# Optimization experiments

Hardware: AMD Instinct MI355X
Metric: run time of the kernel (lower is better)

Reference implementation:

```python
import jax, jax.numpy as jnp
import numpy as np

KK = 9  # 3x3 kernel taps
BN_EPS = 1e-5


def setup_inputs() -> dict:
    key = jax.random.key(0)
    ks = jax.random.split(key, 8)
    B, C, H, W = 2, 64, 256, 256
    O = 64
    x = jax.random.normal(ks[0], (B, C, H, W), dtype=jnp.float32)
    # offset/mask conv: 3*KK output channels (dy[9], dx[9], mask[9])
    w_off = jax.random.normal(ks[1], (3 * KK, C, 3, 3), dtype=jnp.float32) * 0.05
    b_off = jnp.zeros((3 * KK,), dtype=jnp.float32)
    # deformable conv weight
    w = jax.random.normal(ks[2], (O, C, 3, 3), dtype=jnp.float32) * (1.0 / np.sqrt(C * KK))
    b = jnp.zeros((O,), dtype=jnp.float32)
    gamma = jnp.ones((O,), dtype=jnp.float32)
    beta = jnp.zeros((O,), dtype=jnp.float32)
    return {"x": x, "w_off": w_off, "b_off": b_off, "w": w, "b": b,
            "gamma": gamma, "beta": beta}


def _dcn_bn_act_res(x, w_off, b_off, w, b, gamma, beta):
    B, C, H, W = x.shape
    O = w.shape[0]
    # offset/mask prediction via plain 3x3 conv
    om = jax.lax.conv_general_dilated(
        x, w_off, window_strides=(1, 1), padding=[(1, 1), (1, 1)],
        dimension_numbers=("NCHW", "OIHW", "NCHW")) + b_off[None, :, None, None]
    off_y = om[:, :KK]            # [B,9,H,W]
    off_x = om[:, KK:2 * KK]      # [B,9,H,W]
    mask = jax.nn.sigmoid(om[:, 2 * KK:])  # [B,9,H,W] modulation

    # absolute sampling coordinates: base grid + kernel tap offset (-1..1) + learned offset
    ky, kx = jnp.meshgrid(jnp.arange(3), jnp.arange(3), indexing="ij")
    ky = ky.reshape(KK).astype(jnp.float32) - 1.0
    kx = kx.reshape(KK).astype(jnp.float32) - 1.0
    hs = jnp.arange(H, dtype=jnp.float32)
    ws = jnp.arange(W, dtype=jnp.float32)
    py = off_y + hs[None, None, :, None] + ky[None, :, None, None]  # [B,9,H,W]
    px = off_x + ws[None, None, None, :] + kx[None, :, None, None]

    y0 = jnp.floor(py)
    x0 = jnp.floor(px)
    wy = py - y0
    wx = px - x0
    y0i = y0.astype(jnp.int32)
    x0i = x0.astype(jnp.int32)

    def gather(img, yi, xi):
        # img [C,H,W], yi/xi [9,H,W]; zero outside (implicit zero padding)
        valid = (yi >= 0) & (yi < H) & (xi >= 0) & (xi < W)
        yc = jnp.clip(yi, 0, H - 1)
        xc = jnp.clip(xi, 0, W - 1)
        return img[:, yc, xc] * valid[None].astype(img.dtype)  # [C,9,H,W]

    def sample_one(img, yi, xi, wy_, wx_):
        v00 = gather(img, yi, xi)
        v01 = gather(img, yi, xi + 1)
        v10 = gather(img, yi + 1, xi)
        v11 = gather(img, yi + 1, xi + 1)
        w00 = ((1 - wy_) * (1 - wx_))[None]
        w01 = ((1 - wy_) * wx_)[None]
        w10 = (wy_ * (1 - wx_))[None]
        w11 = (wy_ * wx_)[None]
        return v00 * w00 + v01 * w01 + v10 * w10 + v11 * w11  # [C,9,H,W]

    sampled = jax.vmap(sample_one)(x, y0i, x0i, wy, wx)  # [B,C,9,H,W]
    sampled = sampled * mask[:, None]

    out = jnp.einsum("bckhw,ock->bohw", sampled, w.reshape(O, C, KK))
    out = out + b[None, :, None, None]

    # BatchNorm (training-mode batch statistics)
    mu = out.mean(axis=(0, 2, 3), keepdims=True)
    var = out.var(axis=(0, 2, 3), keepdims=True)
    out = (out - mu) * jax.lax.rsqrt(var + BN_EPS)
    out = out * gamma[None, :, None, None] + beta[None, :, None, None]

    return jax.nn.relu(out) + x  # residual


def reference(x, w_off, b_off, w, b, gamma, beta):
    return _dcn_bn_act_res(x, w_off, b_off, w, b, gamma, beta)
```

## Files before the change

kernel.cpp:

```cpp
#include <hip/hip_runtime.h>
#include <hip/hip_fp16.h>
#include <math.h>

#define HWSZ 65536
#define IMGH 256
#define IMGW 256

typedef _Float16 half8 __attribute__((ext_vector_type(8)));
typedef float f32x4 __attribute__((ext_vector_type(4)));

__device__ inline unsigned short f2bf(float f) {
    unsigned u = __float_as_uint(f);
    return (unsigned short)((u + 0x7fffu + ((u >> 16) & 1u)) >> 16);
}
__device__ inline unsigned short f2h(float f) {
    __half h = __float2half(f);
    return __half_as_ushort(h);
}
__device__ inline __half2 duph2(unsigned s) {
    union { unsigned u; __half2 h; } c;
    c.u = (s & 0xffffu) * 0x10001u;
    return c.h;
}
__device__ inline void hacc(const uint4& q, __half2 w, __half2* v) {
    const __half2* h = (const __half2*)&q;
    v[0] = __hfma2(h[0], w, v[0]);
    v[1] = __hfma2(h[1], w, v[1]);
    v[2] = __hfma2(h[2], w, v[2]);
    v[3] = __hfma2(h[3], w, v[3]);
}

__global__ void prep_weights(const float* __restrict__ w_off,
                             const float* __restrict__ w,
                             unsigned short* __restrict__ wApack,
                             unsigned short* __restrict__ wOffPack) {
    int i = blockIdx.x * 256 + threadIdx.x;
    if (i < 36864) {
        int e = i;
        int j = e & 7, lane = (e >> 3) & 63, kk = (e >> 9) & 1;
        int t2 = e >> 10;
        int tap = t2 % 9, g = t2 / 9;
        int o = g * 16 + (lane & 15);
        int c = kk * 32 + ((lane >> 4) & 3) * 8 + j;
        wApack[e] = f2h(w[(o * 64 + c) * 9 + tap]);
    } else if (i < 36864 + 18432) {
        int e = i - 36864;
        int j = e & 7, lane = (e >> 3) & 63, kk = (e >> 9) & 1;
        int t2 = e >> 10;
        int tap = t2 % 9, mt = t2 / 9;
        int d = mt * 16 + (lane & 15);
        int c = kk * 32 + ((lane >> 4) & 3) * 8 + j;
        float v = (d < 27) ? w_off[(d * 64 + c) * 9 + tap] : 0.f;
        wOffPack[e] = f2h(v);
    }
}

__global__ __launch_bounds__(256) void transpose_x(const float* __restrict__ x,
                                                   unsigned short* __restrict__ xT) {
    __shared__ float tile[64 * 65];
    int blk = blockIdx.x;
    int b = blk >> 10;
    int p0 = (blk & 1023) * 64;
    int t = threadIdx.x;
    const float* xb = x + (size_t)b * 64 * HWSZ;
    unsigned short* xTb = xT + (size_t)b * HWSZ * 64;
    int pp = t & 63;
    int c0r = t >> 6;
#pragma unroll
    for (int i = 0; i < 16; ++i) {
        int c = c0r + 4 * i;
        tile[c * 65 + pp] = xb[(size_t)c * HWSZ + p0 + pp];
    }
    __syncthreads();
#pragma unroll
    for (int it = 0; it < 2; ++it) {
        int item = t + it * 256;
        int p = item >> 3;
        int c0 = (item & 7) * 8;
        uint4 ow;
        ow.x = f2h(tile[(c0 + 0) * 65 + p]) | ((unsigned)f2h(tile[(c0 + 1) * 65 + p]) << 16);
        ow.y = f2h(tile[(c0 + 2) * 65 + p]) | ((unsigned)f2h(tile[(c0 + 3) * 65 + p]) << 16);
        ow.z = f2h(tile[(c0 + 4) * 65 + p]) | ((unsigned)f2h(tile[(c0 + 5) * 65 + p]) << 16);
        ow.w = f2h(tile[(c0 + 6) * 65 + p]) | ((unsigned)f2h(tile[(c0 + 7) * 65 + p]) << 16);
        *(uint4*)&xTb[(size_t)(p0 + p) * 64 + c0] = ow;
    }
}

__global__ __launch_bounds__(256) void offset_conv(const unsigned short* __restrict__ xT,
                                                   const unsigned short* __restrict__ wOffPack,
                                                   const float* __restrict__ b_off,
                                                   float* __restrict__ om) {
    __shared__ uint4 haloBuf[800];
    char* halo = (char*)haloBuf;
    int bid = blockIdx.x;
    int blk = ((bid & 7) << 8) | (bid >> 3);
    int b = blk >> 10;
    int tb = blk & 1023;
    int ty = tb >> 5, tx = tb & 31;
    int h0 = ty * 8, w0 = tx * 8;
    int t = threadIdx.x;
    const char* xbb = (const char*)(xT + (size_t)b * HWSZ * 64);

    for (int i = t; i < 800; i += 256) {
        int cell = i >> 3;
        int c0 = (i & 7) * 8;
        int r = cell / 10, s = cell - r * 10;
        int y = h0 - 1 + r, xx = w0 - 1 + s;
        uint4 v = {0u, 0u, 0u, 0u};
        if (y >= 0 && y < IMGH && xx >= 0 && xx < IMGW)
            v = *(const uint4*)(xbb + ((size_t)(y * IMGW + xx) << 7) + (c0 << 1));
        *(uint4*)(halo + (cell << 7) + (((c0 << 1)) ^ ((cell & 7) << 4))) = v;
    }
    __syncthreads();

    int lane = t & 63;
    int wid = __builtin_amdgcn_readfirstlane(t >> 6);
    int mt = wid & 1;
    int np = wid >> 1;
    f32x4 z = {0.f, 0.f, 0.f, 0.f};
    f32x4 acc[2] = {z, z};
    int lhi = lane >> 4;

    for (int tap = 0; tap < 9; ++tap) {
        const half8* ap = (const half8*)wOffPack;
        half8 a0 = ap[((mt * 9 + tap) * 2 + 0) * 64 + lane];
        half8 a1 = ap[((mt * 9 + tap) * 2 + 1) * 64 + lane];
        int dy = tap / 3, dx = tap - dy * 3;
#pragma unroll
        for (int nn = 0; nn < 2; ++nn) {
            int p = (np * 2 + nn) * 16 + (lane & 15);
            int cell = ((p >> 3) + dy) * 10 + (p & 7) + dx;
            int base = (cell << 7);
            int swz = (cell & 7) << 4;
            half8 b0 = *(const half8*)(halo + base + ((lhi << 4) ^ swz));
            acc[nn] = __builtin_amdgcn_mfma_f32_16x16x32_f16(a0, b0, acc[nn], 0, 0, 0);
            half8 b1 = *(const half8*)(halo + base + (((4 + lhi) << 4) ^ swz));
            acc[nn] = __builtin_amdgcn_mfma_f32_16x16x32_f16(a1, b1, acc[nn], 0, 0, 0);
        }
    }
    float* omb = om + (size_t)b * 27 * HWSZ;
#pragma unroll
    for (int nn = 0; nn < 2; ++nn) {
#pragma unroll
        for (int jj = 0; jj < 4; ++jj) {
            int d = mt * 16 + lhi * 4 + jj;
            if (d < 27) {
                int p = (np * 2 + nn) * 16 + (lane & 15);
                int gp = (h0 + (p >> 3)) * IMGW + w0 + (p & 7);
                omb[(size_t)d * HWSZ + gp] = acc[nn][jj] + b_off[d];
            }
        }
    }
}

__global__ __launch_bounds__(512, 4) void dcn_main(const unsigned short* __restrict__ xT,
                                                   const float* __restrict__ om,
                                                   const unsigned short* __restrict__ wApack,
                                                   unsigned short* __restrict__ preout,
                                                   float* __restrict__ stats) {
    __shared__ uint4 haloBuf[3744];
    __shared__ unsigned prmi[9][128];
    __shared__ uint2 prmw[9][128];
    __shared__ float bstats[128];
    char* halo = (char*)haloBuf;
    int bid = blockIdx.x;
    int blk = ((bid & 7) << 7) | (bid >> 3);
    int b = blk >> 9;
    int tb = blk & 511;
    int ty = tb >> 5, tx = tb & 31;
    int h0 = ty * 16, w0 = tx * 8;
    int t = threadIdx.x;
    const char* xbb = (const char*)(xT + (size_t)b * HWSZ * 64);
    const float* omb = om + (size_t)b * 27 * HWSZ;
    int lane = t & 63;
    int wid = t >> 6;
    int lp = lane & 15;
    int lhi = lane >> 4;
    int p = wid * 16 + lp;
    int hb = h0 - 5, wb = w0 - 5;

    if (t < 128) bstats[t] = 0.f;

    for (int i = t; i < 3744; i += 512) {
        int cell = i >> 3;
        int ch = i & 7;
        int r = cell / 18, c = cell - r * 18;
        int y = hb + r, xx = wb + c;
        uint4 v = {0u, 0u, 0u, 0u};
        if ((unsigned)y < 256u && (unsigned)xx < 256u)
            v = *(const uint4*)(xbb + ((size_t)((y << 8) + xx) << 7) + (ch << 4));
        *(uint4*)(halo + (cell << 7) + ((ch ^ (cell & 7)) << 4)) = v;
    }

    for (int i = t; i < 1152; i += 512) {
        int tap = i >> 7, pp = i & 127;
        int h = h0 + (pp >> 3), wc = w0 + (pp & 7);
        int gp = h * IMGW + wc;
        float offy = omb[(size_t)tap * HWSZ + gp];
        float offx = omb[(size_t)(tap + 9) * HWSZ + gp];
        float mraw = omb[(size_t)(tap + 18) * HWSZ + gp];
        float m = 1.f / (1.f + __expf(-mraw));
        float pyf = (float)(h + tap / 3 - 1) + offy;
        float pxf = (float)(wc + tap % 3 - 1) + offx;
        float y0f = floorf(pyf), x0f = floorf(pxf);
        float wy = pyf - y0f, wx = pxf - x0f;
        int y0 = (int)y0f, x0 = (int)x0f;
        int y1 = y0 + 1, x1 = x0 + 1;
        float vy0 = (y0 >= 0 && y0 < IMGH) ? 1.f : 0.f;
        float vy1 = (y1 >= 0 && y1 < IMGH) ? 1.f : 0.f;
        float vx0 = (x0 >= 0 && x0 < IMGW) ? 1.f : 0.f;
        float vx1 = (x1 >= 0 && x1 < IMGW) ? 1.f : 0.f;
        float w00 = (1.f - wy) * (1.f - wx) * m * vy0 * vx0;
        float w01 = (1.f - wy) * wx * m * vy0 * vx1;
        float w10 = wy * (1.f - wx) * m * vy1 * vx0;
        float w11 = wy * wx * m * vy1 * vx1;
        prmw[tap][pp] = make_uint2((unsigned)f2h(w00) | ((unsigned)f2h(w01) << 16),
                                   (unsigned)f2h(w10) | ((unsigned)f2h(w11) << 16));
        int ry0 = y0 - hb, rx0 = x0 - wb;
        unsigned enc;
        if ((unsigned)ry0 <= 24u && (unsigned)rx0 <= 16u) {
            enc = (unsigned)((ry0 * 18 + rx0) << 7);
        } else {
            int y0s = min(max(y0, -8), 383) + 8;
            int x0s = min(max(x0, -8), 383) + 8;
            enc = 1u | ((unsigned)y0s << 1) | ((unsigned)x0s << 10);
        }
        prmi[tap][pp] = enc;
    }
    __syncthreads();

    f32x4 z = {0.f, 0.f, 0.f, 0.f};
    f32x4 acc[4] = {z, z, z, z};
    const half8* ap = (const half8*)wApack;
    uint4 q[4][2];

#define LOADC(PI)                                                             \
    {                                                                         \
        unsigned pi_ = (PI);                                                  \
        bool fb_ = (pi_ & 1u);                                                \
        unsigned base_ = fb_ ? 0u : pi_;                                      \
        unsigned o00 = base_, o01 = base_ + 128u,                             \
                 o10 = base_ + 2304u, o11 = base_ + 2432u;                    \
        q[0][0] = *(const uint4*)(halo + o00 + ((lhi ^ ((o00 >> 7) & 7)) << 4));       \
        q[0][1] = *(const uint4*)(halo + o00 + (((4 + lhi) ^ ((o00 >> 7) & 7)) << 4)); \
        q[1][0] = *(const uint4*)(halo + o01 + ((lhi ^ ((o01 >> 7) & 7)) << 4));       \
        q[1][1] = *(const uint4*)(halo + o01 + (((4 + lhi) ^ ((o01 >> 7) & 7)) << 4)); \
        q[2][0] = *(const uint4*)(halo + o10 + ((lhi ^ ((o10 >> 7) & 7)) << 4));       \
        q[2][1] = *(const uint4*)(halo + o10 + (((4 + lhi) ^ ((o10 >> 7) & 7)) << 4)); \
        q[3][0] = *(const uint4*)(halo + o11 + ((lhi ^ ((o11 >> 7) & 7)) << 4));       \
        q[3][1] = *(const uint4*)(halo + o11 + (((4 + lhi) ^ ((o11 >> 7) & 7)) << 4)); \
        if (__ballot(fb_)) {                                                  \
            if (fb_) {                                                        \
                int y0r = (int)((pi_ >> 1) & 511) - 8;                        \
                int x0r = (int)((pi_ >> 10) & 511) - 8;                       \
                int y0c = min(max(y0r, 0), 255), y1c = min(max(y0r + 1, 0), 255); \
                int x0c = min(max(x0r, 0), 255), x1c = min(max(x0r + 1, 0), 255); \
                const char* g00 = xbb + (((y0c << 8) + x0c) << 7) + (lhi << 4); \
                const char* g01 = xbb + (((y0c << 8) + x1c) << 7) + (lhi << 4); \
                const char* g10 = xbb + (((y1c << 8) + x0c) << 7) + (lhi << 4); \
                const char* g11 = xbb + (((y1c << 8) + x1c) << 7) + (lhi << 4); \
                q[0][0] = *(const uint4*)g00; q[0][1] = *(const uint4*)(g00 + 64); \
                q[1][0] = *(const uint4*)g01; q[1][1] = *(const uint4*)(g01 + 64); \
                q[2][0] = *(const uint4*)g10; q[2][1] = *(const uint4*)(g10 + 64); \
                q[3][0] = *(const uint4*)g11; q[3][1] = *(const uint4*)(g11 + 64); \
            }                                                                 \
        }                                                                     \
    }

    unsigned pi = prmi[0][p];
    uint2 ww = prmw[0][p];
    LOADC(pi);

#pragma unroll
    for (int tap = 0; tap < 9; ++tap) {
        __half2 W00 = duph2(ww.x), W01 = duph2(ww.x >> 16);
        __half2 W10 = duph2(ww.y), W11 = duph2(ww.y >> 16);
        union HV { __half2 h2[4]; half8 h8; } V0, V1;
        __half2 z2 = __float2half2_rn(0.f);
#pragma unroll
        for (int j = 0; j < 4; ++j) { V0.h2[j] = z2; V1.h2[j] = z2; }
        hacc(q[0][0], W00, V0.h2); hacc(q[0][1], W00, V1.h2);
        hacc(q[1][0], W01, V0.h2); hacc(q[1][1], W01, V1.h2);
        hacc(q[2][0], W10, V0.h2); hacc(q[2][1], W10, V1.h2);
        hacc(q[3][0], W11, V0.h2); hacc(q[3][1], W11, V1.h2);
        half8 b0 = V0.h8, b1 = V1.h8;
        if (tap < 8) {
            pi = prmi[tap + 1][p];
            ww = prmw[tap + 1][p];
            LOADC(pi);
        }
        __builtin_amdgcn_s_setprio(1);
#pragma unroll
        for (int g2 = 0; g2 < 4; ++g2) {
            half8 a0 = ap[((g2 * 9 + tap) * 2 + 0) * 64 + lane];
            half8 a1 = ap[((g2 * 9 + tap) * 2 + 1) * 64 + lane];
            acc[g2] = __builtin_amdgcn_mfma_f32_16x16x32_f16(a0, b0, acc[g2], 0, 0, 0);
            acc[g2] = __builtin_amdgcn_mfma_f32_16x16x32_f16(a1, b1, acc[g2], 0, 0, 0);
        }
        __builtin_amdgcn_s_setprio(0);
    }
#undef LOADC

    unsigned short* pob = preout + (size_t)b * 64 * HWSZ;
    int gp = (h0 + (p >> 3)) * IMGW + w0 + (p & 7);
#pragma unroll
    for (int g2 = 0; g2 < 4; ++g2) {
#pragma unroll
        for (int jj = 0; jj < 4; ++jj) {
            int o = g2 * 16 + lhi * 4 + jj;
            pob[(size_t)o * HWSZ + gp] = f2bf(acc[g2][jj]);
        }
    }
#pragma unroll
    for (int g2 = 0; g2 < 4; ++g2) {
#pragma unroll
        for (int jj = 0; jj < 4; ++jj) {
            float s1 = acc[g2][jj];
            float s2 = s1 * s1;
#pragma unroll
            for (int mask = 1; mask < 16; mask <<= 1) {
                s1 += __shfl_xor(s1, mask);
                s2 += __shfl_xor(s2, mask);
            }
            if (lp == 0) {
                int o = g2 * 16 + lhi * 4 + jj;
                atomicAdd(&bstats[o], s1);
                atomicAdd(&bstats[64 + o], s2);
            }
        }
    }
    __syncthreads();
    if (t < 128) atomicAdd(&stats[t], bstats[t]);
}

__global__ __launch_bounds__(256) void bn_finalize(const float* __restrict__ stats,
                                                   const float* __restrict__ gamma,
                                                   const float* __restrict__ beta,
                                                   const float* __restrict__ x,
                                                   const unsigned short* __restrict__ preout,
                                                   float* __restrict__ out) {
    int i = blockIdx.x * 256 + threadIdx.x;
    int e0 = i * 8;
    int o = (e0 >> 16) & 63;
    const float inv_n = 1.f / 131072.f;
    float mean = stats[o] * inv_n;
    float var = stats[64 + o] * inv_n - mean * mean;
    float rstd = rsqrtf(var + 1e-5f);
    float g = gamma[o] * rstd;
    float bb = beta[o] - mean * g;
    uint4 q = ((const uint4*)preout)[i];
    float4 x0 = ((const float4*)x)[i * 2];
    float4 x1 = ((const float4*)x)[i * 2 + 1];
    float4 r0, r1;
    r0.x = fmaxf(__uint_as_float(q.x << 16) * g + bb, 0.f) + x0.x;
    r0.y = fmaxf(__uint_as_float(q.x & 0xffff0000u) * g + bb, 0.f) + x0.y;
    r0.z = fmaxf(__uint_as_float(q.y << 16) * g + bb, 0.f) + x0.z;
    r0.w = fmaxf(__uint_as_float(q.y & 0xffff0000u) * g + bb, 0.f) + x0.w;
    r1.x = fmaxf(__uint_as_float(q.z << 16) * g + bb, 0.f) + x1.x;
    r1.y = fmaxf(__uint_as_float(q.z & 0xffff0000u) * g + bb, 0.f) + x1.y;
    r1.z = fmaxf(__uint_as_float(q.w << 16) * g + bb, 0.f) + x1.z;
    r1.w = fmaxf(__uint_as_float(q.w & 0xffff0000u) * g + bb, 0.f) + x1.w;
    ((float4*)out)[i * 2] = r0;
    ((float4*)out)[i * 2 + 1] = r1;
}

extern "C" void kernel_launch(void* const* d_in, const int* in_sizes, int n_in,
                              void* d_out, int out_size, void* d_ws, size_t ws_size,
                              hipStream_t stream) {
    const float* x     = (const float*)d_in[0];
    const float* w_off = (const float*)d_in[1];
    const float* b_off = (const float*)d_in[2];
    const float* w     = (const float*)d_in[3];
    const float* gamma = (const float*)d_in[5];
    const float* beta  = (const float*)d_in[6];
    float* out = (float*)d_out;
    char* wsb = (char*)d_ws;

    unsigned short* xT       = (unsigned short*)wsb;
    float*          om       = (float*)(wsb + 16777216);
    unsigned short* preout   = (unsigned short*)(wsb + 30932992);
    unsigned short* wApack   = (unsigned short*)(wsb + 47710208);
    unsigned short* wOffPack = (unsigned short*)(wsb + 47783936);
    float*          stats    = (float*)(wsb + 47820800);

    hipMemsetAsync(stats, 0, 512, stream);
    prep_weights<<<216, 256, 0, stream>>>(w_off, w, wApack, wOffPack);
    transpose_x<<<2048, 256, 0, stream>>>(x, xT);
    offset_conv<<<2048, 256, 0, stream>>>(xT, wOffPack, b_off, om);
    dcn_main<<<1024, 512, 0, stream>>>(xT, om, wApack, preout, stats);
    bn_finalize<<<4096, 256, 0, stream>>>(stats, gamma, beta, x, preout, out);
}
```

Baseline: 101.6 us.

## Fuse offset/mask convolution into main DCN kernel using the shared halo tile

Removes the separate offset_conv kernel and computes the 27-channel offset/mask conv inside dcn_main from the already-loaded 5-pixel halo, writing results to shared memory instead of a global om buffer. Per-pixel sampling indices and bilinear weights are now held in registers (9 entries per thread) rather than in shared arrays, and halo addressing is simplified to a cell index with XOR swizzle. This eliminates a kernel launch and a ~14MB global round trip for om, at the cost of extra registers and MFMA work inside the main kernel, which may reduce occupancy.

Result: slower. 104.1 us (+2.4%).

```diff
diff --git a/kernel.cpp b/kernel.cpp
--- a/kernel.cpp
+++ b/kernel.cpp
@@ -86,81 +86,14 @@
     }
 }
 
-__global__ __launch_bounds__(256) void offset_conv(const unsigned short* __restrict__ xT,
+__global__ __launch_bounds__(512, 4) void dcn_main(const unsigned short* __restrict__ xT,
+                                                   const unsigned short* __restrict__ wApack,
                                                    const unsigned short* __restrict__ wOffPack,
                                                    const float* __restrict__ b_off,
-                                                   float* __restrict__ om) {
-    __shared__ uint4 haloBuf[800];
-    char* halo = (char*)haloBuf;
-    int bid = blockIdx.x;
-    int blk = ((bid & 7) << 8) | (bid >> 3);
-    int b = blk >> 10;
-    int tb = blk & 1023;
-    int ty = tb >> 5, tx = tb & 31;
-    int h0 = ty * 8, w0 = tx * 8;
-    int t = threadIdx.x;
-    const char* xbb = (const char*)(xT + (size_t)b * HWSZ * 64);
-
-    for (int i = t; i < 800; i += 256) {
-        int cell = i >> 3;
-        int c0 = (i & 7) * 8;
-        int r = cell / 10, s = cell - r * 10;
-        int y = h0 - 1 + r, xx = w0 - 1 + s;
-        uint4 v = {0u, 0u, 0u, 0u};
-        if (y >= 0 && y < IMGH && xx >= 0 && xx < IMGW)
-            v = *(const uint4*)(xbb + ((size_t)(y * IMGW + xx) << 7) + (c0 << 1));
-        *(uint4*)(halo + (cell << 7) + (((c0 << 1)) ^ ((cell & 7) << 4))) = v;
-    }
-    __syncthreads();
-
-    int lane = t & 63;
-    int wid = __builtin_amdgcn_readfirstlane(t >> 6);
-    int mt = wid & 1;
-    int np = wid >> 1;
-    f32x4 z = {0.f, 0.f, 0.f, 0.f};
-    f32x4 acc[2] = {z, z};
-    int lhi = lane >> 4;
-
-    for (int tap = 0; tap < 9; ++tap) {
-        const half8* ap = (const half8*)wOffPack;
-        half8 a0 = ap[((mt * 9 + tap) * 2 + 0) * 64 + lane];
-        half8 a1 = ap[((mt * 9 + tap) * 2 + 1) * 64 + lane];
-        int dy = tap / 3, dx = tap - dy * 3;
-#pragma unroll
-        for (int nn = 0; nn < 2; ++nn) {
-            int p = (np * 2 + nn) * 16 + (lane & 15);
-            int cell = ((p >> 3) + dy) * 10 + (p & 7) + dx;
-            int base = (cell << 7);
-            int swz = (cell & 7) << 4;
-            half8 b0 = *(const half8*)(halo + base + ((lhi << 4) ^ swz));
-            acc[nn] = __builtin_amdgcn_mfma_f32_16x16x32_f16(a0, b0, acc[nn], 0, 0, 0);
-            half8 b1 = *(const half8*)(halo + base + (((4 + lhi) << 4) ^ swz));
-            acc[nn] = __builtin_amdgcn_mfma_f32_16x16x32_f16(a1, b1, acc[nn], 0, 0, 0);
-        }
-    }
-    float* omb = om + (size_t)b * 27 * HWSZ;
-#pragma unroll
-    for (int nn = 0; nn < 2; ++nn) {
-#pragma unroll
-        for (int jj = 0; jj < 4; ++jj) {
-            int d = mt * 16 + lhi * 4 + jj;
-            if (d < 27) {
-                int p = (np * 2 + nn) * 16 + (lane & 15);
-                int gp = (h0 + (p >> 3)) * IMGW + w0 + (p & 7);
-                omb[(size_t)d * HWSZ + gp] = acc[nn][jj] + b_off[d];
-            }
-        }
-    }
-}
-
-__global__ __launch_bounds__(512, 4) void dcn_main(const unsigned short* __restrict__ xT,
-                                                   const float* __restrict__ om,
-                                                   const unsigned short* __restrict__ wApack,
                                                    unsigned short* __restrict__ preout,
                                                    float* __restrict__ stats) {
     __shared__ uint4 haloBuf[3744];
-    __shared__ unsigned prmi[9][128];
-    __shared__ uint2 prmw[9][128];
+    __shared__ float om_s[27 * 128];
     __shared__ float bstats[128];
     char* halo = (char*)haloBuf;
     int bid = blockIdx.x;
@@ -171,11 +104,11 @@
     int h0 = ty * 16, w0 = tx * 8;
     int t = threadIdx.x;
     const char* xbb = (const char*)(xT + (size_t)b * HWSZ * 64);
-    const float* omb = om + (size_t)b * 27 * HWSZ;
     int lane = t & 63;
     int wid = t >> 6;
     int lp = lane & 15;
     int lhi = lane >> 4;
+    unsigned lhi16 = (unsigned)(lhi << 4);
     int p = wid * 16 + lp;
     int hb = h0 - 5, wb = w0 - 5;
 
@@ -191,68 +124,101 @@
             v = *(const uint4*)(xbb + ((size_t)((y << 8) + xx) << 7) + (ch << 4));
         *(uint4*)(halo + (cell << 7) + ((ch ^ (cell & 7)) << 4)) = v;
     }
-
-    for (int i = t; i < 1152; i += 512) {
-        int tap = i >> 7, pp = i & 127;
-        int h = h0 + (pp >> 3), wc = w0 + (pp & 7);
-        int gp = h * IMGW + wc;
-        float offy = omb[(size_t)tap * HWSZ + gp];
-        float offx = omb[(size_t)(tap + 9) * HWSZ + gp];
-        float mraw = omb[(size_t)(tap + 18) * HWSZ + gp];
-        float m = 1.f / (1.f + __expf(-mraw));
-        float pyf = (float)(h + tap / 3 - 1) + offy;
-        float pxf = (float)(wc + tap % 3 - 1) + offx;
-        float y0f = floorf(pyf), x0f = floorf(pxf);
-        float wy = pyf - y0f, wx = pxf - x0f;
-        int y0 = (int)y0f, x0 = (int)x0f;
-        int y1 = y0 + 1, x1 = x0 + 1;
-        float vy0 = (y0 >= 0 && y0 < IMGH) ? 1.f : 0.f;
-        float vy1 = (y1 >= 0 && y1 < IMGH) ? 1.f : 0.f;
-        float vx0 = (x0 >= 0 && x0 < IMGW) ? 1.f : 0.f;
-        float vx1 = (x1 >= 0 && x1 < IMGW) ? 1.f : 0.f;
-        float w00 = (1.f - wy) * (1.f - wx) * m * vy0 * vx0;
-        float w01 = (1.f - wy) * wx * m * vy0 * vx1;
-        float w10 = wy * (1.f - wx) * m * vy1 * vx0;
-        float w11 = wy * wx * m * vy1 * vx1;
-        prmw[tap][pp] = make_uint2((unsigned)f2h(w00) | ((unsigned)f2h(w01) << 16),
-                                   (unsigned)f2h(w10) | ((unsigned)f2h(w11) << 16));
-        int ry0 = y0 - hb, rx0 = x0 - wb;
-        unsigned enc;
-        if ((unsigned)ry0 <= 24u && (unsigned)rx0 <= 16u) {
-            enc = (unsigned)((ry0 * 18 + rx0) << 7);
-        } else {
-            int y0s = min(max(y0, -8), 383) + 8;
-            int x0s = min(max(x0, -8), 383) + 8;
-            enc = 1u | ((unsigned)y0s << 1) | ((unsigned)x0s << 10);
-        }
-        prmi[tap][pp] = enc;
-    }
     __syncthreads();
+
+    {
+        int mt = wid & 1;
+        const half8* wp = (const half8*)wOffPack;
+        f32x4 z0 = {0.f, 0.f, 0.f, 0.f};
+#pragma unroll
+        for (int hf = 0; hf < 2; ++hf) {
+            int nt = (wid >> 1) + hf * 4;
+            int pp = nt * 16 + lp;
+            int pr = pp >> 3, pc = pp & 7;
+            f32x4 oa = z0;
+#pragma unroll
+            for (int tap = 0; tap < 9; ++tap) {
+                int dy = tap / 3, dx = tap - dy * 3;
+                int cell = (pr + dy + 4) * 18 + (pc + dx + 4);
+                unsigned ad = (((unsigned)cell << 7) | (((unsigned)cell & 7) << 4)) ^ lhi16;
+                half8 b0 = *(const half8*)(halo + ad);
+                half8 b1 = *(const half8*)(halo + (ad ^ 64u));
+                half8 wa0 = wp[((mt * 9 + tap) * 2 + 0) * 64 + lane];
+                half8 wa1 = wp[((mt * 9 + tap) * 2 + 1) * 64 + lane];
+                oa = __builtin_amdgcn_mfma_f32_16x16x32_f16(wa0, b0, oa, 0, 0, 0);
+                oa = __builtin_amdgcn_mfma_f32_16x16x32_f16(wa1, b1, oa, 0, 0, 0);
+            }
+#pragma unroll
+            for (int jj = 0; jj < 4; ++jj) {
+                int d = mt * 16 + lhi * 4 + jj;
+                if (d < 27) om_s[d * 128 + pp] = oa[jj] + b_off[d];
+            }
+        }
+    }
+    __syncthreads();
+
+    unsigned enc[9];
+    uint2 wwr[9];
+    {
+        int h = h0 + (p >> 3), wc = w0 + (p & 7);
+#pragma unroll
+        for (int tap = 0; tap < 9; ++tap) {
+            float offy = om_s[tap * 128 + p];
+            float offx = om_s[(tap + 9) * 128 + p];
+            float mraw = om_s[(tap + 18) * 128 + p];
+            float m = 1.f / (1.f + __expf(-mraw));
+            float pyf = (float)(h + tap / 3 - 1) + offy;
+            float pxf = (float)(wc + tap % 3 - 1) + offx;
+            float y0f = floorf(pyf), x0f = floorf(pxf);
+            float wy = pyf - y0f, wx = pxf - x0f;
+            int y0 = (int)y0f, x0 = (int)x0f;
+            int y1 = y0 + 1, x1 = x0 + 1;
+            float vy0 = (y0 >= 0 && y0 < IMGH) ? 1.f : 0.f;
+            float vy1 = (y1 >= 0 && y1 < IMGH) ? 1.f : 0.f;
+            float vx0 = (x0 >= 0 && x0 < IMGW) ? 1.f : 0.f;
+            float vx1 = (x1 >= 0 && x1 < IMGW) ? 1.f : 0.f;
+            float w00 = (1.f - wy) * (1.f - wx) * m * vy0 * vx0;
+            float w01 = (1.f - wy) * wx * m * vy0 * vx1;
+            float w10 = wy * (1.f - wx) * m * vy1 * vx0;
+            float w11 = wy * wx * m * vy1 * vx1;
+            wwr[tap] = make_uint2((unsigned)f2h(w00) | ((unsigned)f2h(w01) << 16),
+                                  (unsigned)f2h(w10) | ((unsigned)f2h(w11) << 16));
+            int ry0 = y0 - hb, rx0 = x0 - wb;
+            if ((unsigned)ry0 <= 24u && (unsigned)rx0 <= 16u) {
+                enc[tap] = (unsigned)(ry0 * 18 + rx0) << 1;
+            } else {
+                int y0s = min(max(y0, -8), 383) + 8;
+                int x0s = min(max(x0, -8), 383) + 8;
+                enc[tap] = 1u | ((unsigned)y0s << 1) | ((unsigned)x0s << 10);
+            }
+        }
+    }
 
     f32x4 z = {0.f, 0.f, 0.f, 0.f};
     f32x4 acc[4] = {z, z, z, z};
     const half8* ap = (const half8*)wApack;
     uint4 q[4][2];
 
-#define LOADC(PI)                                                             \
+#define SBASE(CC) ((((CC) << 7) | (((CC) & 7u) << 4)) ^ lhi16)
+#define LOADC(E)                                                              \
     {                                                                         \
-        unsigned pi_ = (PI);                                                  \
-        bool fb_ = (pi_ & 1u);                                                \
-        unsigned base_ = fb_ ? 0u : pi_;                                      \
-        unsigned o00 = base_, o01 = base_ + 128u,                             \
-                 o10 = base_ + 2304u, o11 = base_ + 2432u;                    \
-        q[0][0] = *(const uint4*)(halo + o00 + ((lhi ^ ((o00 >> 7) & 7)) << 4));       \
-        q[0][1] = *(const uint4*)(halo + o00 + (((4 + lhi) ^ ((o00 >> 7) & 7)) << 4)); \
-        q[1][0] = *(const uint4*)(halo + o01 + ((lhi ^ ((o01 >> 7) & 7)) << 4));       \
-        q[1][1] = *(const uint4*)(halo + o01 + (((4 + lhi) ^ ((o01 >> 7) & 7)) << 4)); \
-        q[2][0] = *(const uint4*)(halo + o10 + ((lhi ^ ((o10 >> 7) & 7)) << 4));       \
-        q[2][1] = *(const uint4*)(halo + o10 + (((4 + lhi) ^ ((o10 >> 7) & 7)) << 4)); \
-        q[3][0] = *(const uint4*)(halo + o11 + ((lhi ^ ((o11 >> 7) & 7)) << 4));       \
-        q[3][1] = *(const uint4*)(halo + o11 + (((4 + lhi) ^ ((o11 >> 7) & 7)) << 4)); \
+        unsigned e_ = (E);                                                    \
+        bool fb_ = (e_ & 1u);                                                 \
+        unsigned cl_ = fb_ ? 0u : (e_ >> 1);                                  \
+        unsigned a00 = SBASE(cl_), a01 = SBASE(cl_ + 1u);                     \
+        unsigned a10 = SBASE(cl_ + 18u), a11 = SBASE(cl_ + 19u);              \
+        q[0][0] = *(const uint4*)(halo + a00);                                \
+        q[0][1] = *(const uint4*)(halo + (a00 ^ 64u));                        \
+        q[1][0] = *(const uint4*)(halo + a01);                                \
+        q[1][1] = *(const uint4*)(halo + (a01 ^ 64u));                        \
+        q[2][0] = *(const uint4*)(halo + a10);                                \
+        q[2][1] = *(const uint4*)(halo + (a10 ^ 64u));                        \
+        q[3][0] = *(const uint4*)(halo + a11);                                \
+        q[3][1] = *(const uint4*)(halo + (a11 ^ 64u));                        \
         if (__ballot(fb_)) {                                                  \
             if (fb_) {                                                        \
-                int y0r = (int)((pi_ >> 1) & 511) - 8;                        \
-                int x0r = (int)((pi_ >> 10) & 511) - 8;                       \
+                int y0r = (int)((e_ >> 1) & 511) - 8;                         \
+                int x0r = (int)((e_ >> 10) & 511) - 8;                        \
                 int y0c = min(max(y0r, 0), 255), y1c = min(max(y0r + 1, 0), 255); \
                 int x0c = min(max(x0r, 0), 255), x1c = min(max(x0r + 1, 0), 255); \
                 const char* g00 = xbb + (((y0c << 8) + x0c) << 7) + (lhi << 4); \
@@ -267,12 +233,11 @@
         }                                                                     \
     }
 
-    unsigned pi = prmi[0][p];
-    uint2 ww = prmw[0][p];
-    LOADC(pi);
+    LOADC(enc[0]);
 
 #pragma unroll
     for (int tap = 0; tap < 9; ++tap) {
+        uint2 ww = wwr[tap];
         __half2 W00 = duph2(ww.x), W01 = duph2(ww.x >> 16);
         __half2 W10 = duph2(ww.y), W11 = duph2(ww.y >> 16);
         union HV { __half2 h2[4]; half8 h8; } V0, V1;
@@ -284,11 +249,7 @@
         hacc(q[2][0], W10, V0.h2); hacc(q[2][1], W10, V1.h2);
         hacc(q[3][0], W11, V0.h2); hacc(q[3][1], W11, V1.h2);
         half8 b0 = V0.h8, b1 = V1.h8;
-        if (tap < 8) {
-            pi = prmi[tap + 1][p];
-            ww = prmw[tap + 1][p];
-            LOADC(pi);
-        }
+        if (tap < 8) LOADC(enc[tap + 1]);
         __builtin_amdgcn_s_setprio(1);
 #pragma unroll
         for (int g2 = 0; g2 < 4; ++g2) {
@@ -300,6 +261,7 @@
         __builtin_amdgcn_s_setprio(0);
     }
 #undef LOADC
+#undef SBASE
 
     unsigned short* pob = preout + (size_t)b * 64 * HWSZ;
     int gp = (h0 + (p >> 3)) * IMGW + w0 + (p & 7);
@@ -377,16 +339,14 @@
     char* wsb = (char*)d_ws;
 
     unsigned short* xT       = (unsigned short*)wsb;
-    float*          om       = (float*)(wsb + 16777216);
-    unsigned short* preout   = (unsigned short*)(wsb + 30932992);
-    unsigned short* wApack   = (unsigned short*)(wsb + 47710208);
-    unsigned short* wOffPack = (unsigned short*)(wsb + 47783936);
-    float*          stats    = (float*)(wsb + 47820800);
+    unsigned short* preout   = (unsigned short*)(wsb + 16777216);
+    unsigned short* wApack   = (unsigned short*)(wsb + 33554432);
+    unsigned short* wOffPack = (unsigned short*)(wsb + 33628160);
+    float*          stats    = (float*)(wsb + 33665024);
 
     hipMemsetAsync(stats, 0, 512, stream);
     prep_weights<<<216, 256, 0, stream>>>(w_off, w, wApack, wOffPack);
     transpose_x<<<2048, 256, 0, stream>>>(x, xT);
-    offset_conv<<<2048, 256, 0, stream>>>(xT, wOffPack, b_off, om);
-    dcn_main<<<1024, 512, 0, stream>>>(xT, om, wApack, preout, stats);
+    dcn_main<<<1024, 512, 0, stream>>>(xT, wApack, wOffPack, b_off, preout, stats);
     bn_finalize<<<4096, 256, 0, stream>>>(stats, gamma, beta, x, preout, out);
 }
```
